# Optimization experiments

Measured on AMD Instinct MI355X. Metric: run time of the kernel, lower is better.

Reference implementation:

```python
import jax, jax.numpy as jnp
import numpy as np

N = 100000
H = 512
NUM_HEADS = 8
G = 512  # number of graphs (segments)


def seg_softmax(s, batch, num_segments):
    # numerically stable segment softmax (PyG-style, +1e-16 in denom)
    m = jax.ops.segment_max(s, batch, num_segments=num_segments)
    e = jnp.exp(s - m[batch])
    d = jax.ops.segment_sum(e, batch, num_segments=num_segments)
    return e / (d[batch] + 1e-16)


def setup_inputs() -> dict:
    key = jax.random.key(0)
    ks = jax.random.split(key, 12)
    s = 0.02
    x = jax.random.normal(ks[0], (N, H), dtype=jnp.float32)
    batch = jnp.sort(jax.random.randint(ks[1], (N,), 0, G)).astype(jnp.int64)
    # GlobalAttention.gate_nn: Linear(H, H//2) -> ReLU -> Linear(H//2, 1)
    ga_g_w1 = jax.random.normal(ks[2], (H, H // 2), dtype=jnp.float32) * s
    ga_g_b1 = jnp.zeros((H // 2,), dtype=jnp.float32)
    ga_g_w2 = jax.random.normal(ks[3], (H // 2, 1), dtype=jnp.float32) * s
    ga_g_b2 = jnp.zeros((1,), dtype=jnp.float32)
    # GlobalAttention.nn: Linear(H, H) -> ReLU
    ga_n_w = jax.random.normal(ks[4], (H, H), dtype=jnp.float32) * s
    ga_n_b = jnp.zeros((H,), dtype=jnp.float32)
    # outer gate_nn: Linear(H, H) -> ReLU -> (Dropout: identity in eval) -> Linear(H, NUM_HEADS)
    g_w1 = jax.random.normal(ks[5], (H, H), dtype=jnp.float32) * s
    g_b1 = jnp.zeros((H,), dtype=jnp.float32)
    g_w2 = jax.random.normal(ks[6], (H, NUM_HEADS), dtype=jnp.float32) * s
    g_b2 = jnp.zeros((NUM_HEADS,), dtype=jnp.float32)
    return dict(x=x, batch=batch,
                ga_g_w1=ga_g_w1, ga_g_b1=ga_g_b1, ga_g_w2=ga_g_w2, ga_g_b2=ga_g_b2,
                ga_n_w=ga_n_w, ga_n_b=ga_n_b,
                g_w1=g_w1, g_b1=g_b1, g_w2=g_w2, g_b2=g_b2)


def reference(x, batch, ga_g_w1, ga_g_b1, ga_g_w2, ga_g_b2, ga_n_w, ga_n_b,
              g_w1, g_b1, g_w2, g_b2):
    # --- GlobalAttention pooling ---
    h = jax.nn.relu(x @ ga_g_w1 + ga_g_b1)          # (N, H//2)
    gate = (h @ ga_g_w2 + ga_g_b2)[:, 0]            # (N,)
    gate = seg_softmax(gate, batch, G)              # segment softmax per graph
    xt = jax.nn.relu(x @ ga_n_w + ga_n_b)           # (N, H)
    graph_embedding = jax.ops.segment_sum(gate[:, None] * xt, batch,
                                          num_segments=G)  # (G, H)
    # --- interpretable attention weights ---
    g = jax.nn.relu(x @ g_w1 + g_b1)                # (N, H); dropout = identity (eval)
    scores = (g @ g_w2 + g_b2).mean(axis=-1)        # (N,) mean over heads
    attention = seg_softmax(scores, batch, G)       # (N,)
    return graph_embedding, attention
```

## Files before the change

kernel.cpp:

```cpp
#include <hip/hip_runtime.h>

#define NN 100000
#define HH 512
#define GG 512
#define NPACK 1280
#define NSTRIP 40
#define SB 32768
#define XTROWS (NN + 128)

typedef unsigned short u16;
typedef __bf16 bf16x8 __attribute__((ext_vector_type(8)));
typedef unsigned short u16x8 __attribute__((ext_vector_type(8)));
typedef float f32x4 __attribute__((ext_vector_type(4)));
typedef __attribute__((address_space(1))) void gvoid_t;
typedef __attribute__((address_space(3))) void lvoid_t;

__device__ __forceinline__ u16 f2bf(float f) {
    unsigned u = __float_as_uint(f);
    unsigned r = u + 0x7FFFu + ((u >> 16) & 1u);
    return (u16)(r >> 16);
}
__device__ __forceinline__ float bf2f(u16 b) {
    return __uint_as_float(((unsigned)b) << 16);
}

__global__ void k_prep(const float* __restrict__ gw1, const float* __restrict__ gb1,
                       const float* __restrict__ gw2v,
                       const float* __restrict__ nw, const float* __restrict__ nb,
                       const float* __restrict__ aw1, const float* __restrict__ ab1,
                       const float* __restrict__ aw2, const int* __restrict__ batch,
                       u16* __restrict__ WT, float* __restrict__ bias, float* __restrict__ wvec,
                       float* __restrict__ out_emb, int* __restrict__ starts) {
    int idx = blockIdx.x * blockDim.x + threadIdx.x;
    int stride = gridDim.x * blockDim.x;
    for (int i = idx; i < NPACK * 512; i += stride) {
        int n = i >> 9, k = i & 511;
        float v;
        if (n < 256)      v = gw1[k * 256 + n];
        else if (n < 768) v = nw[k * 512 + (n - 256)];
        else              v = aw1[k * 512 + (n - 768)];
        int s = n >> 5, nl = n & 31;
        int ck = k >> 3, k3 = k & 7;
        size_t byte = (size_t)s * SB + nl * 1024 + ((size_t)(ck ^ (nl & 15)) << 4) + k3 * 2;
        *(u16*)((char*)WT + byte) = f2bf(v);
    }
    for (int n = idx; n < NPACK; n += stride) {
        float bi, wv;
        if (n < 256)      { bi = gb1[n];       wv = gw2v[n]; }
        else if (n < 768) { bi = nb[n - 256];  wv = 0.f; }
        else {
            bi = ab1[n - 768];
            float s = 0.f;
            for (int h = 0; h < 8; ++h) s += aw2[(n - 768) * 8 + h];
            wv = s * 0.125f;
        }
        bias[n] = bi; wvec[n] = wv;
    }
    for (int i = idx; i < GG * HH; i += stride) out_emb[i] = 0.f;
    for (int g = idx; g <= GG; g += stride) {
        if (g == GG) { starts[GG] = NN; continue; }
        int lo = 0, hi = NN;
        while (lo < hi) { int mid = (lo + hi) >> 1; if (batch[mid] < g) lo = mid + 1; else hi = mid; }
        starts[g] = lo;
    }
}

__global__ __launch_bounds__(128, 1)
void k_gemm(const float* __restrict__ X, const u16* __restrict__ B,
            const float* __restrict__ bias, const float* __restrict__ wvec,
            const float* __restrict__ gb2, const float* __restrict__ ab2,
            u16* __restrict__ xt, float* __restrict__ gs, float* __restrict__ as_) {
    __shared__ __align__(16) char ldsB[2 * SB];

    const int tid = threadIdx.x;
    const int lane = tid & 63;
    const int w = tid >> 6;
    const int m0 = blockIdx.x * 128;
    const int l16 = lane & 15, kq = lane >> 4;

#define STAGE(s, bsel) do {                                                          \
    const char* _src = (const char*)B + (size_t)(s) * SB + tid * 16;                 \
    char* _dst = ldsB + (bsel) * SB + tid * 16;                                      \
    _Pragma("unroll")                                                                \
    for (int _t = 0; _t < 16; ++_t)                                                  \
        __builtin_amdgcn_global_load_lds((gvoid_t*)(_src + _t * 2048),               \
                                         (lvoid_t*)(_dst + _t * 2048), 16, 0, 0);    \
} while (0)

    STAGE(0, 0);

    float b2 = gb2[0];
    float bb = 0.f;
#pragma unroll
    for (int h = 0; h < 8; ++h) bb += ab2[h];
    bb *= 0.125f;

    bf16x8 a_reg[4][16];
#pragma unroll
    for (int i = 0; i < 4; ++i) {
        int row = m0 + w * 64 + i * 16 + l16;
        if (row >= NN) row = NN - 1;
        const float* xp = X + (size_t)row * 512 + kq * 8;
#pragma unroll
        for (int kt = 0; kt < 16; ++kt) {
            float4 f0 = *(const float4*)(xp + kt * 32);
            float4 f1 = *(const float4*)(xp + kt * 32 + 4);
            u16x8 u;
            u[0] = f2bf(f0.x); u[1] = f2bf(f0.y); u[2] = f2bf(f0.z); u[3] = f2bf(f0.w);
            u[4] = f2bf(f1.x); u[5] = f2bf(f1.y); u[6] = f2bf(f1.z); u[7] = f2bf(f1.w);
            a_reg[i][kt] = __builtin_bit_cast(bf16x8, u);
        }
    }

    float sg[4][4], sa[4][4];
#pragma unroll
    for (int i = 0; i < 4; ++i)
#pragma unroll
        for (int r = 0; r < 4; ++r) { sg[i][r] = 0.f; sa[i][r] = 0.f; }

    for (int nt = 0; nt < NSTRIP; ++nt) {
        const int cur = nt & 1;
        if (nt + 1 < NSTRIP) STAGE(nt + 1, cur ^ 1);
        if (nt == NSTRIP - 1)         asm volatile("s_waitcnt vmcnt(0)" ::: "memory");
        else if (nt >= 9 && nt <= 24) asm volatile("s_waitcnt vmcnt(32)" ::: "memory");
        else                          asm volatile("s_waitcnt vmcnt(16)" ::: "memory");
        __builtin_amdgcn_s_barrier();

        f32x4 acc[4][2];
#pragma unroll
        for (int i = 0; i < 4; ++i) { acc[i][0] = {0.f,0.f,0.f,0.f}; acc[i][1] = {0.f,0.f,0.f,0.f}; }

        const char* bbase = ldsB + cur * SB + l16 * 1024;
#pragma unroll
        for (int kt = 0; kt < 16; ++kt) {
            int off = ((kt * 4 + kq) ^ l16) << 4;
            bf16x8 b0 = *(const bf16x8*)(bbase + off);
            bf16x8 b1 = *(const bf16x8*)(bbase + 16384 + off);
#pragma unroll
            for (int i = 0; i < 4; ++i) {
                acc[i][0] = __builtin_amdgcn_mfma_f32_16x16x32_bf16(a_reg[i][kt], b0, acc[i][0], 0, 0, 0);
                acc[i][1] = __builtin_amdgcn_mfma_f32_16x16x32_bf16(a_reg[i][kt], b1, acc[i][1], 0, 0, 0);
            }
        }
        __builtin_amdgcn_s_barrier();

        float bi0 = bias[nt * 32 + l16], bi1 = bias[nt * 32 + 16 + l16];
        if (nt >= 8 && nt < 24) {
            const int sx = nt - 8;
#pragma unroll
            for (int i = 0; i < 4; ++i)
#pragma unroll
                for (int r = 0; r < 4; ++r) {
                    int rg = m0 + w * 64 + i * 16 + kq * 4 + r;
                    ushort2 st;
                    st.x = f2bf(fmaxf(acc[i][0][r] + bi0, 0.f));
                    st.y = f2bf(fmaxf(acc[i][1][r] + bi1, 0.f));
                    *(ushort2*)(xt + (size_t)rg * 512 + sx * 32 + l16 * 2) = st;
                }
        } else {
            float w0 = wvec[nt * 32 + l16], w1 = wvec[nt * 32 + 16 + l16];
            if (nt < 8) {
#pragma unroll
                for (int i = 0; i < 4; ++i)
#pragma unroll
                    for (int r = 0; r < 4; ++r)
                        sg[i][r] += fmaxf(acc[i][0][r] + bi0, 0.f) * w0
                                  + fmaxf(acc[i][1][r] + bi1, 0.f) * w1;
            } else {
#pragma unroll
                for (int i = 0; i < 4; ++i)
#pragma unroll
                    for (int r = 0; r < 4; ++r)
                        sa[i][r] += fmaxf(acc[i][0][r] + bi0, 0.f) * w0
                                  + fmaxf(acc[i][1][r] + bi1, 0.f) * w1;
            }
        }
    }
#undef STAGE

#pragma unroll
    for (int i = 0; i < 4; ++i)
#pragma unroll
        for (int r = 0; r < 4; ++r) {
            float pg = sg[i][r], pa = sa[i][r];
            pg += __shfl_xor(pg, 1); pg += __shfl_xor(pg, 2);
            pg += __shfl_xor(pg, 4); pg += __shfl_xor(pg, 8);
            pa += __shfl_xor(pa, 1); pa += __shfl_xor(pa, 2);
            pa += __shfl_xor(pa, 4); pa += __shfl_xor(pa, 8);
            int rg = m0 + w * 64 + i * 16 + kq * 4 + r;
            if (l16 == 0 && rg < NN) {
                gs[rg] = pg + b2;
                as_[rg] = pa + bb;
            }
        }
}

__global__ void k_seg(const float* __restrict__ gs, const float* __restrict__ as_,
                      const int* __restrict__ starts,
                      float* __restrict__ mg, float* __restrict__ dg,
                      float* __restrict__ ma, float* __restrict__ da) {
    int g = blockIdx.x;
    int s0 = starts[g], s1 = starts[g + 1];
    int tid = threadIdx.x, lane = tid & 63, w = tid >> 6;
    __shared__ float red[8];
    float lmg = -3.0e38f, lma = -3.0e38f;
    for (int i = s0 + tid; i < s1; i += 256) {
        lmg = fmaxf(lmg, gs[i]); lma = fmaxf(lma, as_[i]);
    }
    for (int o = 32; o; o >>= 1) {
        lmg = fmaxf(lmg, __shfl_xor(lmg, o));
        lma = fmaxf(lma, __shfl_xor(lma, o));
    }
    if (lane == 0) { red[w] = lmg; red[4 + w] = lma; }
    __syncthreads();
    float Mg = fmaxf(fmaxf(red[0], red[1]), fmaxf(red[2], red[3]));
    float Ma = fmaxf(fmaxf(red[4], red[5]), fmaxf(red[6], red[7]));
    __syncthreads();
    float sgv = 0.f, sav = 0.f;
    for (int i = s0 + tid; i < s1; i += 256) {
        sgv += expf(gs[i] - Mg); sav += expf(as_[i] - Ma);
    }
    for (int o = 32; o; o >>= 1) { sgv += __shfl_xor(sgv, o); sav += __shfl_xor(sav, o); }
    if (lane == 0) { red[w] = sgv; red[4 + w] = sav; }
    __syncthreads();
    if (tid == 0) {
        mg[g] = Mg; ma[g] = Ma;
        dg[g] = red[0] + red[1] + red[2] + red[3];
        da[g] = red[4] + red[5] + red[6] + red[7];
    }
}

__global__ void k_final(const float* __restrict__ gs, const float* __restrict__ as_,
                        const int* __restrict__ batch,
                        const float* __restrict__ mg, const float* __restrict__ dg,
                        const float* __restrict__ ma, const float* __restrict__ da,
                        float* __restrict__ gate, float* __restrict__ attn) {
    int stride = gridDim.x * blockDim.x;
    for (int i = blockIdx.x * blockDim.x + threadIdx.x; i < NN; i += stride) {
        int b = batch[i];
        gate[i] = expf(gs[i] - mg[b]) / (dg[b] + 1e-16f);
        attn[i] = expf(as_[i] - ma[b]) / (da[b] + 1e-16f);
    }
}

__global__ void k_emb(const u16* __restrict__ xt, const float* __restrict__ gate,
                      const int* __restrict__ starts, float* __restrict__ out) {
    int g = blockIdx.y;
    int part = blockIdx.x;
    int s0 = starts[g], s1 = starts[g + 1];
    int len = s1 - s0;
    int p0 = s0 + (len * part) / 4, p1 = s0 + (len * (part + 1)) / 4;
    int c2 = threadIdx.x;
    int col0 = (c2 >> 4) * 32 + (c2 & 15);
    float a0 = 0.f, a1 = 0.f;
    for (int n = p0; n < p1; ++n) {
        float gn = gate[n];
        ushort2 u = reinterpret_cast<const ushort2*>(xt + (size_t)n * 512)[c2];
        a0 += gn * bf2f(u.x);
        a1 += gn * bf2f(u.y);
    }
    atomicAdd(&out[g * 512 + col0], a0);
    atomicAdd(&out[g * 512 + col0 + 16], a1);
}

extern "C" void kernel_launch(void* const* d_in, const int* in_sizes, int n_in,
                              void* d_out, int out_size, void* d_ws, size_t ws_size,
                              hipStream_t stream) {
    const float* x       = (const float*)d_in[0];
    const int*   batch   = (const int*)d_in[1];
    const float* ga_g_w1 = (const float*)d_in[2];
    const float* ga_g_b1 = (const float*)d_in[3];
    const float* ga_g_w2 = (const float*)d_in[4];
    const float* ga_g_b2 = (const float*)d_in[5];
    const float* ga_n_w  = (const float*)d_in[6];
    const float* ga_n_b  = (const float*)d_in[7];
    const float* g_w1    = (const float*)d_in[8];
    const float* g_b1    = (const float*)d_in[9];
    const float* g_w2    = (const float*)d_in[10];
    const float* g_b2    = (const float*)d_in[11];

    float* out_emb = (float*)d_out;
    float* out_att = out_emb + GG * HH;

    char* p = (char*)d_ws;
    size_t off = 0;
    auto alloc = [&](size_t bytes) -> char* {
        char* q = p + off;
        off += (bytes + 255) & ~(size_t)255;
        return q;
    };
    u16*   xt    = (u16*)  alloc((size_t)XTROWS * HH * 2);
    u16*   WT    = (u16*)  alloc((size_t)NPACK * 512 * 2);
    float* bias  = (float*)alloc(NPACK * 4);
    float* wvec  = (float*)alloc(NPACK * 4);
    float* gs    = (float*)alloc((size_t)NN * 4);
    float* as_   = (float*)alloc((size_t)NN * 4);
    float* gate  = (float*)alloc((size_t)NN * 4);
    float* mg    = (float*)alloc(GG * 4);
    float* dg    = (float*)alloc(GG * 4);
    float* ma    = (float*)alloc(GG * 4);
    float* da    = (float*)alloc(GG * 4);
    int*   starts= (int*)  alloc((GG + 1) * 4);

    k_prep<<<2560, 256, 0, stream>>>(ga_g_w1, ga_g_b1, ga_g_w2, ga_n_w, ga_n_b,
                                     g_w1, g_b1, g_w2, batch, WT, bias, wvec, out_emb, starts);
    k_gemm<<<782, 128, 0, stream>>>(x, WT, bias, wvec, ga_g_b2, g_b2, xt, gs, as_);
    k_seg<<<GG, 256, 0, stream>>>(gs, as_, starts, mg, dg, ma, da);
    k_final<<<400, 256, 0, stream>>>(gs, as_, batch, mg, dg, ma, da, gate, out_att);
    k_emb<<<dim3(4, GG), 256, 0, stream>>>(xt, gate, starts, out_emb);
}
```

Baseline: 580.5 us.

## Use four waves per GEMM block with fewer rows each, pack bias/weight vectors

The GEMM block goes from 2 waves covering 64 rows each to 4 waves covering 32 rows each, which halves the A-register footprint and allows two blocks per CU. The LDS staging work is split across 256 threads, and the vmcnt wait thresholds are retuned to match the new per-thread load count. Bias and projection vectors are packed into one float2 array, and the load is hoisted before the staging issue. The aim is more latency hiding from higher occupancy, at the cost of each B tile in LDS being reused by fewer rows per wave and more waves contending for LDS.

```diff
diff --git a/kernel.cpp b/kernel.cpp
--- a/kernel.cpp
+++ b/kernel.cpp
@@ -29,7 +29,7 @@
                        const float* __restrict__ nw, const float* __restrict__ nb,
                        const float* __restrict__ aw1, const float* __restrict__ ab1,
                        const float* __restrict__ aw2, const int* __restrict__ batch,
-                       u16* __restrict__ WT, float* __restrict__ bias, float* __restrict__ wvec,
+                       u16* __restrict__ WT, float2* __restrict__ bwv,
                        float* __restrict__ out_emb, int* __restrict__ starts) {
     int idx = blockIdx.x * blockDim.x + threadIdx.x;
     int stride = gridDim.x * blockDim.x;
@@ -54,7 +54,7 @@
             for (int h = 0; h < 8; ++h) s += aw2[(n - 768) * 8 + h];
             wv = s * 0.125f;
         }
-        bias[n] = bi; wvec[n] = wv;
+        bwv[n] = make_float2(bi, wv);
     }
     for (int i = idx; i < GG * HH; i += stride) out_emb[i] = 0.f;
     for (int g = idx; g <= GG; g += stride) {
@@ -65,9 +65,9 @@
     }
 }
 
-__global__ __launch_bounds__(128, 1)
+__global__ __launch_bounds__(256, 2)
 void k_gemm(const float* __restrict__ X, const u16* __restrict__ B,
-            const float* __restrict__ bias, const float* __restrict__ wvec,
+            const float2* __restrict__ bwv,
             const float* __restrict__ gb2, const float* __restrict__ ab2,
             u16* __restrict__ xt, float* __restrict__ gs, float* __restrict__ as_) {
     __shared__ __align__(16) char ldsB[2 * SB];
@@ -82,9 +82,9 @@
     const char* _src = (const char*)B + (size_t)(s) * SB + tid * 16;                 \
     char* _dst = ldsB + (bsel) * SB + tid * 16;                                      \
     _Pragma("unroll")                                                                \
-    for (int _t = 0; _t < 16; ++_t)                                                  \
-        __builtin_amdgcn_global_load_lds((gvoid_t*)(_src + _t * 2048),               \
-                                         (lvoid_t*)(_dst + _t * 2048), 16, 0, 0);    \
+    for (int _t = 0; _t < 8; ++_t)                                                   \
+        __builtin_amdgcn_global_load_lds((gvoid_t*)(_src + _t * 4096),               \
+                                         (lvoid_t*)(_dst + _t * 4096), 16, 0, 0);    \
 } while (0)
 
     STAGE(0, 0);
@@ -95,10 +95,10 @@
     for (int h = 0; h < 8; ++h) bb += ab2[h];
     bb *= 0.125f;
 
-    bf16x8 a_reg[4][16];
-#pragma unroll
-    for (int i = 0; i < 4; ++i) {
-        int row = m0 + w * 64 + i * 16 + l16;
+    bf16x8 a_reg[2][16];
+#pragma unroll
+    for (int i = 0; i < 2; ++i) {
+        int row = m0 + w * 32 + i * 16 + l16;
         if (row >= NN) row = NN - 1;
         const float* xp = X + (size_t)row * 512 + kq * 8;
 #pragma unroll
@@ -112,23 +112,29 @@
         }
     }
 
-    float sg[4][4], sa[4][4];
-#pragma unroll
-    for (int i = 0; i < 4; ++i)
+    float sg[2][4], sa[2][4];
+#pragma unroll
+    for (int i = 0; i < 2; ++i)
 #pragma unroll
         for (int r = 0; r < 4; ++r) { sg[i][r] = 0.f; sa[i][r] = 0.f; }
 
     for (int nt = 0; nt < NSTRIP; ++nt) {
         const int cur = nt & 1;
+
+        float2 bw0 = bwv[nt * 32 + l16];
+        float2 bw1 = bwv[nt * 32 + 16 + l16];
+
         if (nt + 1 < NSTRIP) STAGE(nt + 1, cur ^ 1);
+
         if (nt == NSTRIP - 1)         asm volatile("s_waitcnt vmcnt(0)" ::: "memory");
-        else if (nt >= 9 && nt <= 24) asm volatile("s_waitcnt vmcnt(32)" ::: "memory");
-        else                          asm volatile("s_waitcnt vmcnt(16)" ::: "memory");
+        else if (nt >= 9 && nt <= 24) asm volatile("s_waitcnt vmcnt(18)" ::: "memory");
+        else                          asm volatile("s_waitcnt vmcnt(10)" ::: "memory");
         __builtin_amdgcn_s_barrier();
-
-        f32x4 acc[4][2];
-#pragma unroll
-        for (int i = 0; i < 4; ++i) { acc[i][0] = {0.f,0.f,0.f,0.f}; acc[i][1] = {0.f,0.f,0.f,0.f}; }
+        __builtin_amdgcn_sched_barrier(0);
+
+        f32x4 acc[2][2];
+#pragma unroll
+        for (int i = 0; i < 2; ++i) { acc[i][0] = {0.f,0.f,0.f,0.f}; acc[i][1] = {0.f,0.f,0.f,0.f}; }
 
         const char* bbase = ldsB + cur * SB + l16 * 1024;
 #pragma unroll
@@ -137,49 +143,45 @@
             bf16x8 b0 = *(const bf16x8*)(bbase + off);
             bf16x8 b1 = *(const bf16x8*)(bbase + 16384 + off);
 #pragma unroll
-            for (int i = 0; i < 4; ++i) {
+            for (int i = 0; i < 2; ++i) {
                 acc[i][0] = __builtin_amdgcn_mfma_f32_16x16x32_bf16(a_reg[i][kt], b0, acc[i][0], 0, 0, 0);
                 acc[i][1] = __builtin_amdgcn_mfma_f32_16x16x32_bf16(a_reg[i][kt], b1, acc[i][1], 0, 0, 0);
             }
         }
         __builtin_amdgcn_s_barrier();
 
-        float bi0 = bias[nt * 32 + l16], bi1 = bias[nt * 32 + 16 + l16];
         if (nt >= 8 && nt < 24) {
             const int sx = nt - 8;
 #pragma unroll
-            for (int i = 0; i < 4; ++i)
+            for (int i = 0; i < 2; ++i)
 #pragma unroll
                 for (int r = 0; r < 4; ++r) {
-                    int rg = m0 + w * 64 + i * 16 + kq * 4 + r;
+                    int rg = m0 + w * 32 + i * 16 + kq * 4 + r;
                     ushort2 st;
-                    st.x = f2bf(fmaxf(acc[i][0][r] + bi0, 0.f));
-                    st.y = f2bf(fmaxf(acc[i][1][r] + bi1, 0.f));
+                    st.x = f2bf(fmaxf(acc[i][0][r] + bw0.x, 0.f));
+                    st.y = f2bf(fmaxf(acc[i][1][r] + bw1.x, 0.f));
                     *(ushort2*)(xt + (size_t)rg * 512 + sx * 32 + l16 * 2) = st;
                 }
+        } else if (nt < 8) {
+#pragma unroll
+            for (int i = 0; i < 2; ++i)
+#pragma unroll
+                for (int r = 0; r < 4; ++r)
+                    sg[i][r] += fmaxf(acc[i][0][r] + bw0.x, 0.f) * bw0.y
+                              + fmaxf(acc[i][1][r] + bw1.x, 0.f) * bw1.y;
         } else {
-            float w0 = wvec[nt * 32 + l16], w1 = wvec[nt * 32 + 16 + l16];
-            if (nt < 8) {
-#pragma unroll
-                for (int i = 0; i < 4; ++i)
-#pragma unroll
-                    for (int r = 0; r < 4; ++r)
-                        sg[i][r] += fmaxf(acc[i][0][r] + bi0, 0.f) * w0
-                                  + fmaxf(acc[i][1][r] + bi1, 0.f) * w1;
-            } else {
-#pragma unroll
-                for (int i = 0; i < 4; ++i)
-#pragma unroll
-                    for (int r = 0; r < 4; ++r)
-                        sa[i][r] += fmaxf(acc[i][0][r] + bi0, 0.f) * w0
-                                  + fmaxf(acc[i][1][r] + bi1, 0.f) * w1;
-            }
+#pragma unroll
+            for (int i = 0; i < 2; ++i)
+#pragma unroll
+                for (int r = 0; r < 4; ++r)
+                    sa[i][r] += fmaxf(acc[i][0][r] + bw0.x, 0.f) * bw0.y
+                              + fmaxf(acc[i][1][r] + bw1.x, 0.f) * bw1.y;
         }
     }
 #undef STAGE
 
 #pragma unroll
-    for (int i = 0; i < 4; ++i)
+    for (int i = 0; i < 2; ++i)
 #pragma unroll
         for (int r = 0; r < 4; ++r) {
             float pg = sg[i][r], pa = sa[i][r];
@@ -187,7 +189,7 @@
             pg += __shfl_xor(pg, 4); pg += __shfl_xor(pg, 8);
             pa += __shfl_xor(pa, 1); pa += __shfl_xor(pa, 2);
             pa += __shfl_xor(pa, 4); pa += __shfl_xor(pa, 8);
-            int rg = m0 + w * 64 + i * 16 + kq * 4 + r;
+            int rg = m0 + w * 32 + i * 16 + kq * 4 + r;
             if (l16 == 0 && rg < NN) {
                 gs[rg] = pg + b2;
                 as_[rg] = pa + bb;
@@ -289,22 +291,21 @@
         off += (bytes + 255) & ~(size_t)255;
         return q;
     };
-    u16*   xt    = (u16*)  alloc((size_t)XTROWS * HH * 2);
-    u16*   WT    = (u16*)  alloc((size_t)NPACK * 512 * 2);
-    float* bias  = (float*)alloc(NPACK * 4);
-    float* wvec  = (float*)alloc(NPACK * 4);
-    float* gs    = (float*)alloc((size_t)NN * 4);
-    float* as_   = (float*)alloc((size_t)NN * 4);
-    float* gate  = (float*)alloc((size_t)NN * 4);
-    float* mg    = (float*)alloc(GG * 4);
-    float* dg    = (float*)alloc(GG * 4);
-    float* ma    = (float*)alloc(GG * 4);
-    float* da    = (float*)alloc(GG * 4);
-    int*   starts= (int*)  alloc((GG + 1) * 4);
+    u16*    xt    = (u16*)   alloc((size_t)XTROWS * HH * 2);
+    u16*    WT    = (u16*)   alloc((size_t)NPACK * 512 * 2);
+    float2* bwv   = (float2*)alloc(NPACK * 8);
+    float*  gs    = (float*) alloc((size_t)NN * 4);
+    float*  as_   = (float*) alloc((size_t)NN * 4);
+    float*  gate  = (float*) alloc((size_t)NN * 4);
+    float*  mg    = (float*) alloc(GG * 4);
+    float*  dg    = (float*) alloc(GG * 4);
+    float*  ma    = (float*) alloc(GG * 4);
+    float*  da    = (float*) alloc(GG * 4);
+    int*    starts= (int*)   alloc((GG + 1) * 4);
 
     k_prep<<<2560, 256, 0, stream>>>(ga_g_w1, ga_g_b1, ga_g_w2, ga_n_w, ga_n_b,
-                                     g_w1, g_b1, g_w2, batch, WT, bias, wvec, out_emb, starts);
-    k_gemm<<<782, 128, 0, stream>>>(x, WT, bias, wvec, ga_g_b2, g_b2, xt, gs, as_);
+                                     g_w1, g_b1, g_w2, batch, WT, bwv, out_emb, starts);
+    k_gemm<<<782, 256, 0, stream>>>(x, WT, bwv, ga_g_b2, g_b2, xt, gs, as_);
     k_seg<<<GG, 256, 0, stream>>>(gs, as_, starts, mg, dg, ma, da);
     k_final<<<400, 256, 0, stream>>>(gs, as_, batch, mg, dg, ma, da, gate, out_att);
     k_emb<<<dim3(4, GG), 256, 0, stream>>>(xt, gate, starts, out_emb);
```

After: 469.7 us. 1.24x faster.
